# Optimization experiments

Hardware: AMD Instinct MI355X
Metric: run time of the kernel (lower is better)

Reference implementation:

```python
import jax, jax.numpy as jnp
import numpy as np

B, S, D = 2, 2048, 2048
H, H_KV, HD = 8, 1, 256   # attention heads, kv heads, head_dim
N_REP = H // H_KV


def setup_inputs() -> dict:
    key = jax.random.key(0)
    ks = jax.random.split(key, 8)
    std = 1.0 / np.sqrt(D)
    return {
        "hidden_states": jax.random.normal(ks[0], (B, S, D), dtype=jnp.float32),
        "attention_mask": jnp.zeros((B, 1, S, S), dtype=jnp.float32),
        "cos": jax.random.uniform(ks[1], (B, S, HD), dtype=jnp.float32),
        "sin": jax.random.uniform(ks[2], (B, S, HD), dtype=jnp.float32),
        "Wq": jax.random.normal(ks[3], (D, H * HD), dtype=jnp.float32) * std,
        "Wk": jax.random.normal(ks[4], (D, H_KV * HD), dtype=jnp.float32) * std,
        "Wv": jax.random.normal(ks[5], (D, H_KV * HD), dtype=jnp.float32) * std,
        "Wo": jax.random.normal(ks[6], (H * HD, D), dtype=jnp.float32) * std,
    }


def _rotate_half(x):
    x1, x2 = jnp.split(x, 2, axis=-1)
    return jnp.concatenate((-x2, x1), axis=-1)


def reference(hidden_states, attention_mask, cos, sin, Wq, Wk, Wv, Wo):
    b, s, _ = hidden_states.shape
    # projections -> [b, heads, s, hd]
    q = (hidden_states @ Wq).reshape(b, s, H, HD).transpose(0, 2, 1, 3)
    k = (hidden_states @ Wk).reshape(b, s, H_KV, HD).transpose(0, 2, 1, 3)
    v = (hidden_states @ Wv).reshape(b, s, H_KV, HD).transpose(0, 2, 1, 3)
    # RoPE (unsqueeze_dim=1)
    c = cos[:, None, :, :]
    sn = sin[:, None, :, :]
    q = q * c + _rotate_half(q) * sn
    k = k * c + _rotate_half(k) * sn
    # GQA: repeat kv heads
    k = jnp.repeat(k, N_REP, axis=1)
    v = jnp.repeat(v, N_REP, axis=1)
    # attention
    scores = jnp.einsum("bhqd,bhkd->bhqk", q, k) / jnp.sqrt(jnp.float32(HD))
    scores = scores + attention_mask[:, :, :, :k.shape[2]]
    attn_weights = jax.nn.softmax(scores.astype(jnp.float32), axis=-1).astype(q.dtype)
    # dropout p=0.0 -> identity
    out = jnp.einsum("bhqk,bhkd->bhqd", attn_weights, v)
    out = out.transpose(0, 2, 1, 3).reshape(b, s, H * HD)
    out = out @ Wo
    return out, attn_weights
```

## Files before the change

### kernel.cpp

```cpp
#include <hip/hip_runtime.h>
#include <hip/hip_bf16.h>

typedef float f32x4 __attribute__((ext_vector_type(4)));
typedef short short8 __attribute__((ext_vector_type(8)));
typedef unsigned int uint2v __attribute__((ext_vector_type(2)));

#define DI __device__ __forceinline__

DI unsigned short f2bf(float f) {
  unsigned int u = __float_as_uint(f);
  u += 0x7fffu + ((u >> 16) & 1u);
  return (unsigned short)(u >> 16);
}

DI unsigned int packbf(float a, float b) {
  return (unsigned int)f2bf(a) | ((unsigned int)f2bf(b) << 16);
}

DI void gload16(const unsigned short* g, unsigned short* l) {
  __builtin_amdgcn_global_load_lds((const __attribute__((address_space(1))) void*)g,
                                   (__attribute__((address_space(3))) void*)l, 16, 0, 0);
}

__global__ void cvt_bf16_kernel(const float* __restrict__ src,
                                unsigned short* __restrict__ dst, long n) {
  long i = ((long)blockIdx.x * blockDim.x + threadIdx.x) * 8;
  if (i >= n) return;
  float4 a = *(const float4*)(src + i);
  float4 b = *(const float4*)(src + i + 4);
  short8 v;
  v[0] = f2bf(a.x); v[1] = f2bf(a.y); v[2] = f2bf(a.z); v[3] = f2bf(a.w);
  v[4] = f2bf(b.x); v[5] = f2bf(b.y); v[6] = f2bf(b.z); v[7] = f2bf(b.w);
  *(short8*)(dst + i) = v;
}

__global__ void transpose_cvt_kernel(const float* __restrict__ src,
                                     unsigned short* __restrict__ dst,
                                     int ldsrc, int lddst, long sBatch, long dBatch) {
  __shared__ float tile[32][33];
  const float* s = src + (long)blockIdx.z * sBatch;
  unsigned short* d = dst + (long)blockIdx.z * dBatch;
  int c0 = blockIdx.x * 32, r0 = blockIdx.y * 32;
  int tx = threadIdx.x, ty = threadIdx.y;
#pragma unroll
  for (int k = 0; k < 4; k++)
    tile[ty + 8 * k][tx] = s[(long)(r0 + ty + 8 * k) * ldsrc + c0 + tx];
  __syncthreads();
#pragma unroll
  for (int k = 0; k < 4; k++)
    d[(long)(c0 + ty + 8 * k) * lddst + r0 + tx] = f2bf(tile[tx][ty + 8 * k]);
}

__global__ void transpose_v_kernel(const float* __restrict__ qkv,
                                   unsigned short* __restrict__ VtC) {
  __shared__ float tile[32][33];
  int b = blockIdx.z;
  int d0 = blockIdx.x * 32, s0 = blockIdx.y * 32;
  int tx = threadIdx.x, ty = threadIdx.y;
  const float* s = qkv + (long)b * 2048 * 2560 + 2304;
#pragma unroll
  for (int k = 0; k < 4; k++)
    tile[ty + 8 * k][tx] = s[(long)(s0 + ty + 8 * k) * 2560 + d0 + tx];
  __syncthreads();
  unsigned short* d = VtC + (long)b * 524288 + (long)(s0 >> 5) * 8192;
#pragma unroll
  for (int k = 0; k < 4; k++) {
    int dd = d0 + ty + 8 * k;
    d[dd * 32 + (tx ^ ((dd & 3) << 3))] = f2bf(tile[tx][ty + 8 * k]);
  }
}

__global__ void rope_kernel(const float* __restrict__ qkv, const float* __restrict__ cs,
                            const float* __restrict__ sn, unsigned short* __restrict__ Qb,
                            unsigned short* __restrict__ Ksw) {
  int bid = blockIdx.x;
  int hp = bid % 9;
  int bs = bid / 9;
  int d = threadIdx.x;
  long row = (long)bs * 2560 + hp * 256;
  float x = qkv[row + d];
  float o = (d < 128) ? -qkv[row + d + 128] : qkv[row + d - 128];
  long ci = (long)bs * 256 + d;
  float r = x * cs[ci] + o * sn[ci];
  unsigned short v = f2bf(r);
  if (hp < 8) {
    int b = bs >> 11, s = bs & 2047;
    Qb[((long)(b * 8 + hp) * 2048 + s) * 256 + d] = v;
  } else {
    Ksw[(long)bs * 256 + (d ^ ((bs & 7) << 3))] = v;
  }
}

template <bool AF32, bool CBF16>
__launch_bounds__(256)
__global__ void gemm_bt_kernel(const void* __restrict__ Av,
                               const unsigned short* __restrict__ Btg,
                               void* __restrict__ Cv,
                               int K, int lda, int ldb, int ldc,
                               int zShift, long aBatch, long bBatch, long cBatch, long cHead) {
  __shared__ unsigned short Asm_[128 * 32];
  __shared__ unsigned short Bsm_[128 * 32];
  int z = blockIdx.z;
  int zb = z >> zShift, zh = z - (zb << zShift);
  const unsigned short* Bt = Btg + (long)zb * bBatch;
  const unsigned short* A16 = (const unsigned short*)Av + (long)z * aBatch;
  const float* A32 = (const float*)Av + (long)z * aBatch;
  int m0 = blockIdx.y * 128, n0 = blockIdx.x * 128;
  int tid = threadIdx.x, w = tid >> 6, lane = tid & 63, c = lane & 15, t = lane >> 4;
  int wm = w >> 1, wn = w & 1;
  f32x4 zero4 = {0.f, 0.f, 0.f, 0.f};
  f32x4 acc[4][4];
#pragma unroll
  for (int i = 0; i < 4; i++)
#pragma unroll
    for (int j = 0; j < 4; j++) acc[i][j] = zero4;

  for (int kt = 0; kt < K; kt += 32) {
    if constexpr (!AF32) {
#pragma unroll
      for (int jj = 0; jj < 2; jj++) {
        int slot = (w * 2 + jj) * 64 + lane;
        int r = slot >> 2, g = slot & 3;
        int gs = g ^ ((r >> 1) & 3);
        gload16(A16 + (long)(m0 + r) * lda + kt + gs * 8, Asm_ + slot * 8);
      }
    } else {
#pragma unroll
      for (int jj = 0; jj < 2; jj++) {
        int slot = jj * 256 + tid;
        int r = slot >> 2, g = slot & 3;
        int gs = g ^ ((r >> 1) & 3);
        const float* p = A32 + (long)(m0 + r) * lda + kt + gs * 8;
        float4 x = *(const float4*)p;
        float4 y = *(const float4*)(p + 4);
        short8 v;
        v[0] = f2bf(x.x); v[1] = f2bf(x.y); v[2] = f2bf(x.z); v[3] = f2bf(x.w);
        v[4] = f2bf(y.x); v[5] = f2bf(y.y); v[6] = f2bf(y.z); v[7] = f2bf(y.w);
        *(short8*)(Asm_ + slot * 8) = v;
      }
    }
#pragma unroll
    for (int jj = 0; jj < 2; jj++) {
      int slot = (w * 2 + jj) * 64 + lane;
      int r = slot >> 2, g = slot & 3;
      int gs = g ^ ((r >> 1) & 3);
      gload16(Bt + (long)(n0 + r) * ldb + kt + gs * 8, Bsm_ + slot * 8);
    }
    __syncthreads();
    short8 af[4], bfg[4];
#pragma unroll
    for (int mi = 0; mi < 4; mi++) {
      int r = wm * 64 + mi * 16 + c;
      af[mi] = *(const short8*)(Asm_ + r * 32 + ((t ^ ((r >> 1) & 3)) * 8));
    }
#pragma unroll
    for (int ni = 0; ni < 4; ni++) {
      int r = wn * 64 + ni * 16 + c;
      bfg[ni] = *(const short8*)(Bsm_ + r * 32 + ((t ^ ((r >> 1) & 3)) * 8));
    }
#pragma unroll
    for (int mi = 0; mi < 4; mi++)
#pragma unroll
      for (int ni = 0; ni < 4; ni++)
        acc[mi][ni] = __builtin_amdgcn_mfma_f32_16x16x32_bf16(af[mi], bfg[ni], acc[mi][ni], 0, 0, 0);
    __syncthreads();
  }
  long cOff = (long)zb * cBatch + zh * cHead;
#pragma unroll
  for (int mi = 0; mi < 4; mi++) {
#pragma unroll
    for (int j = 0; j < 4; j++) {
      int row = m0 + wm * 64 + mi * 16 + t * 4 + j;
#pragma unroll
      for (int ni = 0; ni < 4; ni++) {
        int col = n0 + wn * 64 + ni * 16 + c;
        float v = acc[mi][ni][j];
        long idx = cOff + (long)row * ldc + col;
        if constexpr (CBF16) ((unsigned short*)Cv)[idx] = f2bf(v);
        else ((float*)Cv)[idx] = v;
      }
    }
  }
}

#define KC 32
__launch_bounds__(256, 2)
__global__ void attn_fused_kernel(const unsigned short* __restrict__ Qb,
                                  const unsigned short* __restrict__ Ksw,
                                  const unsigned short* __restrict__ VtC,
                                  const float* __restrict__ mask,
                                  float* __restrict__ attnW,
                                  unsigned short* __restrict__ attnO) {
  __shared__ unsigned short Ksm[2][KC * 256];
  __shared__ unsigned short Vsm[2][256 * KC];
  __shared__ unsigned short Pw[4][16 * 32];
  const int id = blockIdx.x;
  const int sw = (id & 7) * 64 + (id >> 3);
  const int qblk = sw & 31, bh = sw >> 5;
  const int b = bh >> 3;
  const int tid = threadIdx.x, w = tid >> 6, lane = tid & 63;
  const int c = lane & 15, t = lane >> 4;
  const int q0w = qblk * 64 + w * 16;
  const float scale = 0.0625f;

  const unsigned short* Qrow = Qb + ((long)bh * 2048 + q0w + c) * 256 + t * 8;
  short8 qf[8];
#pragma unroll
  for (int ks = 0; ks < 8; ks++) qf[ks] = *(const short8*)(Qrow + ks * 32);

  const unsigned short* Kg = Ksw + (long)b * 524288;
  const float* mrow = mask + (long)b * 4194304 + (long)(q0w + c) * 2048 + t * 4;

  float lp = 0.f;

#pragma unroll
  for (int i = 0; i < 4; i++) {
    int slot = i * 256 + tid;
    gload16(Kg + slot * 8, Ksm[0] + slot * 8);
  }
  for (int kc = 0; kc < 64; kc++) {
    int cur = kc & 1;
    __syncthreads();
    if (kc < 63) {
      const unsigned short* src = Kg + (long)(kc + 1) * 8192;
#pragma unroll
      for (int i = 0; i < 4; i++) {
        int slot = i * 256 + tid;
        gload16(src + slot * 8, Ksm[cur ^ 1] + slot * 8);
      }
    }
    f32x4 a0 = {0.f, 0.f, 0.f, 0.f}, a1 = {0.f, 0.f, 0.f, 0.f};
#pragma unroll
    for (int ks = 0; ks < 8; ks++) {
      int g0 = ((ks * 4 + t) ^ (c & 7)) * 8;
      short8 k0 = *(const short8*)(Ksm[cur] + c * 256 + g0);
      short8 k1 = *(const short8*)(Ksm[cur] + (16 + c) * 256 + g0);
      a0 = __builtin_amdgcn_mfma_f32_16x16x32_bf16(k0, qf[ks], a0, 0, 0, 0);
      a1 = __builtin_amdgcn_mfma_f32_16x16x32_bf16(k1, qf[ks], a1, 0, 0, 0);
    }
    const float* mp = mrow + kc * 32;
    f32x4 mv0 = *(const f32x4*)(mp);
    f32x4 mv1 = *(const f32x4*)(mp + 16);
#pragma unroll
    for (int j = 0; j < 4; j++) {
      lp += __expf(a0[j] * scale + mv0[j]);
      lp += __expf(a1[j] * scale + mv1[j]);
    }
  }
  lp += __shfl_xor(lp, 16);
  lp += __shfl_xor(lp, 32);
  float rinv = 1.0f / lp;

  const unsigned short* Vg = VtC + (long)b * 524288;
  float* aWrow = attnW + (long)bh * 4194304 + (long)(q0w + c) * 2048 + t * 4;
  unsigned short* myPw = &Pw[w][0];
  const int pwbase = c * 32;
  f32x4 accO[16];
#pragma unroll
  for (int i = 0; i < 16; i++) accO[i] = (f32x4){0.f, 0.f, 0.f, 0.f};

#pragma unroll
  for (int i = 0; i < 4; i++) {
    int slot = i * 256 + tid;
    gload16(Kg + slot * 8, Ksm[0] + slot * 8);
    gload16(Vg + slot * 8, Vsm[0] + slot * 8);
  }
  for (int kc = 0; kc < 64; kc++) {
    int cur = kc & 1;
    __syncthreads();
    if (kc < 63) {
      const unsigned short* ksrc = Kg + (long)(kc + 1) * 8192;
      const unsigned short* vsrc = Vg + (long)(kc + 1) * 8192;
#pragma unroll
      for (int i = 0; i < 4; i++) {
        int slot = i * 256 + tid;
        gload16(ksrc + slot * 8, Ksm[cur ^ 1] + slot * 8);
        gload16(vsrc + slot * 8, Vsm[cur ^ 1] + slot * 8);
      }
    }
    f32x4 a0 = {0.f, 0.f, 0.f, 0.f}, a1 = {0.f, 0.f, 0.f, 0.f};
#pragma unroll
    for (int ks = 0; ks < 8; ks++) {
      int g0 = ((ks * 4 + t) ^ (c & 7)) * 8;
      short8 k0 = *(const short8*)(Ksm[cur] + c * 256 + g0);
      short8 k1 = *(const short8*)(Ksm[cur] + (16 + c) * 256 + g0);
      a0 = __builtin_amdgcn_mfma_f32_16x16x32_bf16(k0, qf[ks], a0, 0, 0, 0);
      a1 = __builtin_amdgcn_mfma_f32_16x16x32_bf16(k1, qf[ks], a1, 0, 0, 0);
    }
    const float* mp = mrow + kc * 32;
    f32x4 mv0 = *(const f32x4*)(mp);
    f32x4 mv1 = *(const f32x4*)(mp + 16);
    f32x4 p0, p1;
#pragma unroll
    for (int j = 0; j < 4; j++) {
      p0[j] = __expf(a0[j] * scale + mv0[j]) * rinv;
      p1[j] = __expf(a1[j] * scale + mv1[j]) * rinv;
    }
    *(f32x4*)(aWrow + kc * 32) = p0;
    *(f32x4*)(aWrow + kc * 32 + 16) = p1;
    uint2v w0, w1;
    w0[0] = packbf(p0[0], p0[1]); w0[1] = packbf(p0[2], p0[3]);
    w1[0] = packbf(p1[0], p1[1]); w1[1] = packbf(p1[2], p1[3]);
    *(uint2v*)(myPw + pwbase + ((t * 4) ^ ((c & 3) << 3))) = w0;
    *(uint2v*)(myPw + pwbase + ((16 + t * 4) ^ ((c & 3) << 3))) = w1;
    short8 pa = *(const short8*)(myPw + pwbase + ((t * 8) ^ ((c & 3) << 3)));
#pragma unroll
    for (int dt = 0; dt < 16; dt++) {
      int d = dt * 16 + c;
      short8 vf = *(const short8*)(Vsm[cur] + d * 32 + ((t * 8) ^ ((c & 3) << 3)));
      accO[dt] = __builtin_amdgcn_mfma_f32_16x16x32_bf16(pa, vf, accO[dt], 0, 0, 0);
    }
  }
  long obase = ((long)b * 2048 + q0w + t * 4) * 2048 + (bh & 7) * 256 + c;
#pragma unroll
  for (int dt = 0; dt < 16; dt++)
#pragma unroll
    for (int j = 0; j < 4; j++)
      attnO[obase + (long)j * 2048 + dt * 16] = f2bf(accO[dt][j]);
}

extern "C" void kernel_launch(void* const* d_in, const int* in_sizes, int n_in,
                              void* d_out, int out_size, void* d_ws, size_t ws_size,
                              hipStream_t stream) {
  const float* hidden = (const float*)d_in[0];
  const float* mask = (const float*)d_in[1];
  const float* cosb = (const float*)d_in[2];
  const float* sinb = (const float*)d_in[3];
  const float* Wq = (const float*)d_in[4];
  const float* Wk = (const float*)d_in[5];
  const float* Wv = (const float*)d_in[6];
  const float* Wo = (const float*)d_in[7];
  float* out = (float*)d_out;
  float* attnW = out + 8388608;

  char* ws = (char*)d_ws;
  unsigned short* hidB  = (unsigned short*)(ws + 0);
  unsigned short* WqkvT = (unsigned short*)(ws + 16777216);
  unsigned short* WoT   = (unsigned short*)(ws + 27262976);
  float*          qkv   = (float*)(ws + 35651584);
  unsigned short* Qb    = (unsigned short*)(ws + 77594624);
  unsigned short* Ksw   = (unsigned short*)(ws + 94371840);
  unsigned short* VtC   = (unsigned short*)(ws + 96468992);
  unsigned short* attnO = (unsigned short*)(ws + 98566144);

  cvt_bf16_kernel<<<4096, 256, 0, stream>>>(hidden, hidB, 8388608L);
  transpose_cvt_kernel<<<dim3(64, 64, 1), dim3(32, 8), 0, stream>>>(Wq, WqkvT, 2048, 2048, 0, 0);
  transpose_cvt_kernel<<<dim3(8, 64, 1), dim3(32, 8), 0, stream>>>(Wk, WqkvT + (long)2048 * 2048, 256, 2048, 0, 0);
  transpose_cvt_kernel<<<dim3(8, 64, 1), dim3(32, 8), 0, stream>>>(Wv, WqkvT + (long)2304 * 2048, 256, 2048, 0, 0);
  transpose_cvt_kernel<<<dim3(64, 64, 1), dim3(32, 8), 0, stream>>>(Wo, WoT, 2048, 2048, 0, 0);
  gemm_bt_kernel<false, false><<<dim3(20, 32, 1), 256, 0, stream>>>(
      hidB, WqkvT, qkv, 2048, 2048, 2048, 2560, 0, 0, 0, 0, 0);
  rope_kernel<<<36864, 256, 0, stream>>>(qkv, cosb, sinb, Qb, Ksw);
  transpose_v_kernel<<<dim3(8, 64, 2), dim3(32, 8), 0, stream>>>(qkv, VtC);
  attn_fused_kernel<<<512, 256, 0, stream>>>(Qb, Ksw, VtC, mask, attnW, attnO);
  gemm_bt_kernel<false, false><<<dim3(16, 32, 1), 256, 0, stream>>>(
      attnO, WoT, out, 2048, 2048, 2048, 2048, 0, 0, 0, 0, 0);
}
```

Measured before the change: 419.3 us.

## Give each attention wave two 16-row query tiles to reuse K/V fragments

The attention block drops from four waves to two, and each wave now handles 32 query rows (two 16-row tiles). Every K and V fragment read from LDS therefore feeds two MFMAs, halving LDS read traffic per unit of compute. The cost is twice the accumulator and Q-fragment registers per wave (32 f32x4 output accumulators plus 16 short8 Q fragments), which risks spills and lower occupancy. Fewer waves per block also leaves less parallelism to hide latency.

New measurement: 476.4 us. 1.14x slower.

```diff
diff --git a/kernel.cpp b/kernel.cpp
--- a/kernel.cpp
+++ b/kernel.cpp
@@ -184,7 +184,7 @@
 }
 
 #define KC 32
-__launch_bounds__(256, 2)
+__launch_bounds__(128, 2)
 __global__ void attn_fused_kernel(const unsigned short* __restrict__ Qb,
                                   const unsigned short* __restrict__ Ksw,
                                   const unsigned short* __restrict__ VtC,
@@ -193,29 +193,36 @@
                                   unsigned short* __restrict__ attnO) {
   __shared__ unsigned short Ksm[2][KC * 256];
   __shared__ unsigned short Vsm[2][256 * KC];
-  __shared__ unsigned short Pw[4][16 * 32];
+  __shared__ unsigned short Pw[2][2][16 * 32];
   const int id = blockIdx.x;
   const int sw = (id & 7) * 64 + (id >> 3);
   const int qblk = sw & 31, bh = sw >> 5;
   const int b = bh >> 3;
   const int tid = threadIdx.x, w = tid >> 6, lane = tid & 63;
   const int c = lane & 15, t = lane >> 4;
-  const int q0w = qblk * 64 + w * 16;
+  const int q0 = qblk * 64 + w * 32;
   const float scale = 0.0625f;
 
-  const unsigned short* Qrow = Qb + ((long)bh * 2048 + q0w + c) * 256 + t * 8;
-  short8 qf[8];
-#pragma unroll
-  for (int ks = 0; ks < 8; ks++) qf[ks] = *(const short8*)(Qrow + ks * 32);
+  short8 qf0[8], qf1[8];
+  {
+    const unsigned short* Qr0 = Qb + ((long)bh * 2048 + q0 + c) * 256 + t * 8;
+    const unsigned short* Qr1 = Qr0 + 16 * 256;
+#pragma unroll
+    for (int ks = 0; ks < 8; ks++) {
+      qf0[ks] = *(const short8*)(Qr0 + ks * 32);
+      qf1[ks] = *(const short8*)(Qr1 + ks * 32);
+    }
+  }
 
   const unsigned short* Kg = Ksw + (long)b * 524288;
-  const float* mrow = mask + (long)b * 4194304 + (long)(q0w + c) * 2048 + t * 4;
-
-  float lp = 0.f;
-
-#pragma unroll
-  for (int i = 0; i < 4; i++) {
-    int slot = i * 256 + tid;
+  const float* mrow0 = mask + (long)b * 4194304 + (long)(q0 + c) * 2048 + t * 4;
+  const float* mrow1 = mrow0 + 16 * 2048;
+
+  float lp0 = 0.f, lp1 = 0.f;
+
+#pragma unroll
+  for (int i = 0; i < 8; i++) {
+    int slot = i * 128 + tid;
     gload16(Kg + slot * 8, Ksm[0] + slot * 8);
   }
   for (int kc = 0; kc < 64; kc++) {
@@ -224,44 +231,53 @@
     if (kc < 63) {
       const unsigned short* src = Kg + (long)(kc + 1) * 8192;
 #pragma unroll
-      for (int i = 0; i < 4; i++) {
-        int slot = i * 256 + tid;
+      for (int i = 0; i < 8; i++) {
+        int slot = i * 128 + tid;
         gload16(src + slot * 8, Ksm[cur ^ 1] + slot * 8);
       }
     }
-    f32x4 a0 = {0.f, 0.f, 0.f, 0.f}, a1 = {0.f, 0.f, 0.f, 0.f};
+    f32x4 a00 = {0.f, 0.f, 0.f, 0.f}, a01 = a00, a10 = a00, a11 = a00;
 #pragma unroll
     for (int ks = 0; ks < 8; ks++) {
       int g0 = ((ks * 4 + t) ^ (c & 7)) * 8;
       short8 k0 = *(const short8*)(Ksm[cur] + c * 256 + g0);
       short8 k1 = *(const short8*)(Ksm[cur] + (16 + c) * 256 + g0);
-      a0 = __builtin_amdgcn_mfma_f32_16x16x32_bf16(k0, qf[ks], a0, 0, 0, 0);
-      a1 = __builtin_amdgcn_mfma_f32_16x16x32_bf16(k1, qf[ks], a1, 0, 0, 0);
-    }
-    const float* mp = mrow + kc * 32;
-    f32x4 mv0 = *(const f32x4*)(mp);
-    f32x4 mv1 = *(const f32x4*)(mp + 16);
+      a00 = __builtin_amdgcn_mfma_f32_16x16x32_bf16(k0, qf0[ks], a00, 0, 0, 0);
+      a01 = __builtin_amdgcn_mfma_f32_16x16x32_bf16(k0, qf1[ks], a01, 0, 0, 0);
+      a10 = __builtin_amdgcn_mfma_f32_16x16x32_bf16(k1, qf0[ks], a10, 0, 0, 0);
+      a11 = __builtin_amdgcn_mfma_f32_16x16x32_bf16(k1, qf1[ks], a11, 0, 0, 0);
+    }
+    const float* mp0 = mrow0 + kc * 32;
+    const float* mp1 = mrow1 + kc * 32;
+    f32x4 m00 = *(const f32x4*)(mp0);
+    f32x4 m10 = *(const f32x4*)(mp0 + 16);
+    f32x4 m01 = *(const f32x4*)(mp1);
+    f32x4 m11 = *(const f32x4*)(mp1 + 16);
 #pragma unroll
     for (int j = 0; j < 4; j++) {
-      lp += __expf(a0[j] * scale + mv0[j]);
-      lp += __expf(a1[j] * scale + mv1[j]);
-    }
-  }
-  lp += __shfl_xor(lp, 16);
-  lp += __shfl_xor(lp, 32);
-  float rinv = 1.0f / lp;
+      lp0 += __expf(a00[j] * scale + m00[j]);
+      lp0 += __expf(a10[j] * scale + m10[j]);
+      lp1 += __expf(a01[j] * scale + m01[j]);
+      lp1 += __expf(a11[j] * scale + m11[j]);
+    }
+  }
+  lp0 += __shfl_xor(lp0, 16); lp0 += __shfl_xor(lp0, 32);
+  lp1 += __shfl_xor(lp1, 16); lp1 += __shfl_xor(lp1, 32);
+  float ri0 = 1.0f / lp0, ri1 = 1.0f / lp1;
 
   const unsigned short* Vg = VtC + (long)b * 524288;
-  float* aWrow = attnW + (long)bh * 4194304 + (long)(q0w + c) * 2048 + t * 4;
-  unsigned short* myPw = &Pw[w][0];
+  float* aW0 = attnW + (long)bh * 4194304 + (long)(q0 + c) * 2048 + t * 4;
+  float* aW1 = aW0 + 16 * 2048;
+  unsigned short* pw0 = &Pw[w][0][0];
+  unsigned short* pw1 = &Pw[w][1][0];
   const int pwbase = c * 32;
-  f32x4 accO[16];
-#pragma unroll
-  for (int i = 0; i < 16; i++) accO[i] = (f32x4){0.f, 0.f, 0.f, 0.f};
-
-#pragma unroll
-  for (int i = 0; i < 4; i++) {
-    int slot = i * 256 + tid;
+  f32x4 accO0[16], accO1[16];
+#pragma unroll
+  for (int i = 0; i < 16; i++) { accO0[i] = (f32x4){0.f, 0.f, 0.f, 0.f}; accO1[i] = accO0[i]; }
+
+#pragma unroll
+  for (int i = 0; i < 8; i++) {
+    int slot = i * 128 + tid;
     gload16(Kg + slot * 8, Ksm[0] + slot * 8);
     gload16(Vg + slot * 8, Vsm[0] + slot * 8);
   }
@@ -272,51 +288,69 @@
       const unsigned short* ksrc = Kg + (long)(kc + 1) * 8192;
       const unsigned short* vsrc = Vg + (long)(kc + 1) * 8192;
 #pragma unroll
-      for (int i = 0; i < 4; i++) {
-        int slot = i * 256 + tid;
+      for (int i = 0; i < 8; i++) {
+        int slot = i * 128 + tid;
         gload16(ksrc + slot * 8, Ksm[cur ^ 1] + slot * 8);
         gload16(vsrc + slot * 8, Vsm[cur ^ 1] + slot * 8);
       }
     }
-    f32x4 a0 = {0.f, 0.f, 0.f, 0.f}, a1 = {0.f, 0.f, 0.f, 0.f};
+    f32x4 a00 = {0.f, 0.f, 0.f, 0.f}, a01 = a00, a10 = a00, a11 = a00;
 #pragma unroll
     for (int ks = 0; ks < 8; ks++) {
       int g0 = ((ks * 4 + t) ^ (c & 7)) * 8;
       short8 k0 = *(const short8*)(Ksm[cur] + c * 256 + g0);
       short8 k1 = *(const short8*)(Ksm[cur] + (16 + c) * 256 + g0);
-      a0 = __builtin_amdgcn_mfma_f32_16x16x32_bf16(k0, qf[ks], a0, 0, 0, 0);
-      a1 = __builtin_amdgcn_mfma_f32_16x16x32_bf16(k1, qf[ks], a1, 0, 0, 0);
-    }
-    const float* mp = mrow + kc * 32;
-    f32x4 mv0 = *(const f32x4*)(mp);
-    f32x4 mv1 = *(const f32x4*)(mp + 16);
-    f32x4 p0, p1;
+      a00 = __builtin_amdgcn_mfma_f32_16x16x32_bf16(k0, qf0[ks], a00, 0, 0, 0);
+      a01 = __builtin_amdgcn_mfma_f32_16x16x32_bf16(k0, qf1[ks], a01, 0, 0, 0);
+      a10 = __builtin_amdgcn_mfma_f32_16x16x32_bf16(k1, qf0[ks], a10, 0, 0, 0);
+      a11 = __builtin_amdgcn_mfma_f32_16x16x32_bf16(k1, qf1[ks], a11, 0, 0, 0);
+    }
+    const float* mp0 = mrow0 + kc * 32;
+    const float* mp1 = mrow1 + kc * 32;
+    f32x4 m00 = *(const f32x4*)(mp0);
+    f32x4 m10 = *(const f32x4*)(mp0 + 16);
+    f32x4 m01 = *(const f32x4*)(mp1);
+    f32x4 m11 = *(const f32x4*)(mp1 + 16);
+    f32x4 p00, p10, p01, p11;
 #pragma unroll
     for (int j = 0; j < 4; j++) {
-      p0[j] = __expf(a0[j] * scale + mv0[j]) * rinv;
-      p1[j] = __expf(a1[j] * scale + mv1[j]) * rinv;
-    }
-    *(f32x4*)(aWrow + kc * 32) = p0;
-    *(f32x4*)(aWrow + kc * 32 + 16) = p1;
-    uint2v w0, w1;
-    w0[0] = packbf(p0[0], p0[1]); w0[1] = packbf(p0[2], p0[3]);
-    w1[0] = packbf(p1[0], p1[1]); w1[1] = packbf(p1[2], p1[3]);
-    *(uint2v*)(myPw + pwbase + ((t * 4) ^ ((c & 3) << 3))) = w0;
-    *(uint2v*)(myPw + pwbase + ((16 + t * 4) ^ ((c & 3) << 3))) = w1;
-    short8 pa = *(const short8*)(myPw + pwbase + ((t * 8) ^ ((c & 3) << 3)));
+      p00[j] = __expf(a00[j] * scale + m00[j]) * ri0;
+      p10[j] = __expf(a10[j] * scale + m10[j]) * ri0;
+      p01[j] = __expf(a01[j] * scale + m01[j]) * ri1;
+      p11[j] = __expf(a11[j] * scale + m11[j]) * ri1;
+    }
+    *(f32x4*)(aW0 + kc * 32) = p00;
+    *(f32x4*)(aW0 + kc * 32 + 16) = p10;
+    *(f32x4*)(aW1 + kc * 32) = p01;
+    *(f32x4*)(aW1 + kc * 32 + 16) = p11;
+    uint2v w00, w10, w01, w11;
+    w00[0] = packbf(p00[0], p00[1]); w00[1] = packbf(p00[2], p00[3]);
+    w10[0] = packbf(p10[0], p10[1]); w10[1] = packbf(p10[2], p10[3]);
+    w01[0] = packbf(p01[0], p01[1]); w01[1] = packbf(p01[2], p01[3]);
+    w11[0] = packbf(p11[0], p11[1]); w11[1] = packbf(p11[2], p11[3]);
+    *(uint2v*)(pw0 + pwbase + ((t * 4) ^ ((c & 3) << 3))) = w00;
+    *(uint2v*)(pw0 + pwbase + ((16 + t * 4) ^ ((c & 3) << 3))) = w10;
+    *(uint2v*)(pw1 + pwbase + ((t * 4) ^ ((c & 3) << 3))) = w01;
+    *(uint2v*)(pw1 + pwbase + ((16 + t * 4) ^ ((c & 3) << 3))) = w11;
+    short8 pa0 = *(const short8*)(pw0 + pwbase + ((t * 8) ^ ((c & 3) << 3)));
+    short8 pa1 = *(const short8*)(pw1 + pwbase + ((t * 8) ^ ((c & 3) << 3)));
 #pragma unroll
     for (int dt = 0; dt < 16; dt++) {
       int d = dt * 16 + c;
       short8 vf = *(const short8*)(Vsm[cur] + d * 32 + ((t * 8) ^ ((c & 3) << 3)));
-      accO[dt] = __builtin_amdgcn_mfma_f32_16x16x32_bf16(pa, vf, accO[dt], 0, 0, 0);
-    }
-  }
-  long obase = ((long)b * 2048 + q0w + t * 4) * 2048 + (bh & 7) * 256 + c;
+      accO0[dt] = __builtin_amdgcn_mfma_f32_16x16x32_bf16(pa0, vf, accO0[dt], 0, 0, 0);
+      accO1[dt] = __builtin_amdgcn_mfma_f32_16x16x32_bf16(pa1, vf, accO1[dt], 0, 0, 0);
+    }
+  }
+  long ob0 = ((long)b * 2048 + q0 + t * 4) * 2048 + (bh & 7) * 256 + c;
+  long ob1 = ob0 + 16 * 2048;
 #pragma unroll
   for (int dt = 0; dt < 16; dt++)
 #pragma unroll
-    for (int j = 0; j < 4; j++)
-      attnO[obase + (long)j * 2048 + dt * 16] = f2bf(accO[dt][j]);
+    for (int j = 0; j < 4; j++) {
+      attnO[ob0 + (long)j * 2048 + dt * 16] = f2bf(accO0[dt][j]);
+      attnO[ob1 + (long)j * 2048 + dt * 16] = f2bf(accO1[dt][j]);
+    }
 }
 
 extern "C" void kernel_launch(void* const* d_in, const int* in_sizes, int n_in,
@@ -352,7 +386,7 @@
       hidB, WqkvT, qkv, 2048, 2048, 2048, 2560, 0, 0, 0, 0, 0);
   rope_kernel<<<36864, 256, 0, stream>>>(qkv, cosb, sinb, Qb, Ksw);
   transpose_v_kernel<<<dim3(8, 64, 2), dim3(32, 8), 0, stream>>>(qkv, VtC);
-  attn_fused_kernel<<<512, 256, 0, stream>>>(Qb, Ksw, VtC, mask, attnW, attnO);
+  attn_fused_kernel<<<512, 128, 0, stream>>>(Qb, Ksw, VtC, mask, attnW, attnO);
   gemm_bt_kernel<false, false><<<dim3(16, 32, 1), 256, 0, stream>>>(
       attnO, WoT, out, 2048, 2048, 2048, 2048, 0, 0, 0, 0, 0);
 }
```
